# Kernel optimization log

Hardware: AMD Instinct MI355X
Metric: run time of the kernel (lower is better)

## Reference

```python
import jax, jax.numpy as jnp
import numpy as np

N_OBJ, N_SR, N_V, N_F = 8192, 4096, 4100, 4096
EPS = 1e-8


def setup_inputs() -> dict:
    key = jax.random.key(0)
    k1, k2, k3, k4, k5 = jax.random.split(key, 5)
    obj_points = jax.random.normal(k1, (N_OBJ, 3), jnp.float32)
    sr_points = 0.5 * jax.random.normal(k2, (N_SR, 3), jnp.float32)
    hand_verts = 0.5 * jax.random.normal(k3, (N_V, 3), jnp.float32)
    face_normals = jax.random.normal(k4, (N_F, 3), jnp.float32)
    hand_faces = jax.random.randint(k5, (N_F, 3), 0, N_V)
    return dict(obj_points=obj_points, sr_points=sr_points,
                hand_verts=hand_verts, face_normals=face_normals,
                hand_faces=hand_faces)


def reference(obj_points, sr_points, hand_verts, face_normals, hand_faces):
    # --- get_NN: brute-force nearest hand point for every object point ---
    d2 = (jnp.sum(obj_points**2, -1)[:, None]
          + jnp.sum(sr_points**2, -1)[None, :]
          - 2.0 * obj_points @ sr_points.T)          # [N, M] squared dists
    nn_idx = jnp.argmin(d2, axis=1)                   # [N]
    trg_pts = sr_points[nn_idx]                       # batched_index_select -> [N,3]
    D = trg_pts - obj_points                          # ray directions [N,3]

    # --- ray-triangle intersection (plane test + 3 edge half-plane tests) ---
    # All [F,N,3] intermediates are avoided via triple-product expansion:
    # every quantity reduces to einsums of per-face [F,3] with per-ray [N,3].
    tri = hand_verts[hand_faces]                      # [F,3,3]
    v0, v1, v2 = tri[:, 0], tri[:, 1], tri[:, 2]
    n = face_normals                                  # [F,3]

    denom = jnp.einsum('fk,nk->fn', n, D)             # D . n   [F,N]
    num = jnp.sum(v0 * n, -1)[:, None] - jnp.einsum('fk,nk->fn', n, obj_points)
    dmask = jnp.abs(denom) > EPS
    t = num / jnp.where(dmask, denom, 1.0)            # plane hit parameter [F,N]

    def edge_sign(va, vb):
        # ((vb-va) x (P-va)) . n  with  P = O + t*D, expanded bilinearly
        c = jnp.cross(n, vb - va)                     # [F,3]
        base = (jnp.einsum('fk,nk->fn', c, obj_points)
                - jnp.sum(va * c, -1)[:, None])
        return base + t * jnp.einsum('fk,nk->fn', c, D)

    inside = ((edge_sign(v0, v1) >= 0)
              & (edge_sign(v1, v2) >= 0)
              & (edge_sign(v2, v0) >= 0))
    hit = inside & dmask & (t > EPS)                  # [F,N]

    hit_number = jnp.sum(hit.astype(jnp.int32), axis=0)   # per ray [N]
    interior = (hit_number % 2) != 0                        # odd parity -> inside

    diff = trg_pts - obj_points
    pen_dist = jnp.sqrt(jnp.sum(diff**2 * interior[:, None].astype(diff.dtype)) + 1e-12)

    # --- contact_map_of_m_to_n(obj_points, sr_points) ---
    nn_dist = jnp.sqrt(jnp.maximum(jnp.min(d2, axis=1), 0.0))
    cmap = 1.0 - 2.0 * (jax.nn.sigmoid(100.0 * nn_dist) - 0.5)

    return pen_dist, cmap
```

## Files before the change

### kernel.cpp

```cpp
#include <hip/hip_runtime.h>
#include <math.h>

#define N_OBJ 8192
#define N_SR  4096
#define N_F   4096
#define EPSF  1e-8f
#define EPS2F 1e-16f

typedef float v2f __attribute__((ext_vector_type(2)));
static __device__ __forceinline__ v2f sp(float x) { v2f r; r.x = x; r.y = x; return r; }
static __device__ __forceinline__ v2f vfma(v2f a, v2f b, v2f c) { return __builtin_elementwise_fma(a, b, c); }

__global__ void __launch_bounds__(256) nn_all(const float* __restrict__ obj,
                                              const float* __restrict__ sr,
                                              const float* __restrict__ hv,
                                              const float* __restrict__ fn,
                                              const int* __restrict__ hf,
                                              float* __restrict__ out,
                                              float4* __restrict__ Dws,
                                              float4* __restrict__ F,
                                              int* __restrict__ done) {
    __shared__ float4 cXY[512];
    __shared__ float4 cZS[512];
    const int tid = threadIdx.x, b = blockIdx.x;
    const float2* sr2 = (const float2*)sr;

    if (b == 0 && tid == 0) done[0] = 0;
    if (tid < 4) {
        const int f = b * 4 + tid;
        const int i0 = hf[3*f], i1 = hf[3*f+1], i2 = hf[3*f+2];
        const float v0x = hv[3*i0], v0y = hv[3*i0+1], v0z = hv[3*i0+2];
        const float v1x = hv[3*i1], v1y = hv[3*i1+1], v1z = hv[3*i1+2];
        const float v2x = hv[3*i2], v2y = hv[3*i2+1], v2z = hv[3*i2+2];
        const float nx = fn[3*f], ny = fn[3*f+1], nz = fn[3*f+2];
        F[4*f+0] = make_float4(nx, ny, nz, v0x*nx + v0y*ny + v0z*nz);
        {
            float ex = v1x-v0x, ey = v1y-v0y, ez = v1z-v0z;
            float cx = ny*ez-nz*ey, cy = nz*ex-nx*ez, cz = nx*ey-ny*ex;
            F[4*f+1] = make_float4(cx, cy, cz, v0x*cx + v0y*cy + v0z*cz);
        }
        {
            float ex = v2x-v1x, ey = v2y-v1y, ez = v2z-v1z;
            float cx = ny*ez-nz*ey, cy = nz*ex-nx*ez, cz = nx*ey-ny*ex;
            F[4*f+2] = make_float4(cx, cy, cz, v1x*cx + v1y*cy + v1z*cz);
        }
        {
            float ex = v0x-v2x, ey = v0y-v2y, ez = v0z-v2z;
            float cx = ny*ez-nz*ey, cy = nz*ex-nx*ez, cz = nx*ey-ny*ex;
            F[4*f+3] = make_float4(cx, cy, cz, v2x*cx + v2y*cy + v2z*cz);
        }
    }

    const int w = tid >> 6, lane = tid & 63;
    const int p0 = b * 8 + w * 2, p1 = p0 + 1;

    const float ax = obj[3*p0], ay = obj[3*p0+1], az = obj[3*p0+2];
    const float bx = obj[3*p1], by = obj[3*p1+1], bz = obj[3*p1+2];
    const float aaa = fmaf(ax, ax, fmaf(ay, ay, az * az));
    const float aab = fmaf(bx, bx, fmaf(by, by, bz * bz));

    float a0 = INFINITY, a1 = INFINITY, c0v = INFINITY, c1v = INFINITY;
    int ai0 = 0, ai1 = 1, ci0 = 0, ci1 = 1;

    for (int c = 0; c < 4; ++c) {
        __syncthreads();
        {
#pragma unroll
            for (int t = 0; t < 2; ++t) {
                int e = t * 256 + tid;
                int gp = c * 512 + e;
                float2 A = sr2[3 * gp], B = sr2[3 * gp + 1], C = sr2[3 * gp + 2];
                float x0 = A.x, y0 = A.y, z0 = B.x, x1 = B.y, y1 = C.x, z1 = C.y;
                cXY[e] = make_float4(x0, x1, y0, y1);
                cZS[e] = make_float4(z0, z1,
                                     fmaf(x0, x0, fmaf(y0, y0, z0 * z0)),
                                     fmaf(x1, x1, fmaf(y1, y1, z1 * z1)));
            }
        }
        __syncthreads();

        int e2 = c * 1024 + lane * 2;
#pragma unroll
        for (int step = 0; step < 8; ++step) {
            int e = step * 64 + lane;
            float4 A = cXY[e];
            float4 B = cZS[e];
            v2f X; X.x = A.x; X.y = A.y;
            v2f Y; Y.x = A.z; Y.y = A.w;
            v2f Z; Z.x = B.x; Z.y = B.y;
            v2f SS; SS.x = B.z; SS.y = B.w;
            {
                v2f d  = vfma(Z, sp(az), vfma(Y, sp(ay), X * sp(ax)));
                v2f d2 = vfma(d, sp(-2.f), SS);
                bool q0 = d2.x < a0, q1 = d2.y < a1;
                a0 = q0 ? d2.x : a0;  ai0 = q0 ? e2     : ai0;
                a1 = q1 ? d2.y : a1;  ai1 = q1 ? e2 + 1 : ai1;
            }
            {
                v2f d  = vfma(Z, sp(bz), vfma(Y, sp(by), X * sp(bx)));
                v2f d2 = vfma(d, sp(-2.f), SS);
                bool q0 = d2.x < c0v, q1 = d2.y < c1v;
                c0v = q0 ? d2.x : c0v;  ci0 = q0 ? e2     : ci0;
                c1v = q1 ? d2.y : c1v;  ci1 = q1 ? e2 + 1 : ci1;
            }
            e2 += 128;
        }
    }

    float bdA = a0; int biA = ai0;
    if (a1 < bdA || (a1 == bdA && ai1 < biA)) { bdA = a1; biA = ai1; }
    float bdB = c0v; int biB = ci0;
    if (c1v < bdB || (c1v == bdB && ci1 < biB)) { bdB = c1v; biB = ci1; }
#pragma unroll
    for (int off = 32; off > 0; off >>= 1) {
        float d = __shfl_down(bdA, off);
        int   i = __shfl_down(biA, off);
        if (d < bdA || (d == bdA && i < biA)) { bdA = d; biA = i; }
        float e = __shfl_down(bdB, off);
        int   j = __shfl_down(biB, off);
        if (e < bdB || (e == bdB && j < biB)) { bdB = e; biB = j; }
    }
    if (lane == 0) {
        {
            float dx = sr[3*biA] - ax, dy = sr[3*biA+1] - ay, dz = sr[3*biA+2] - az;
            Dws[p0] = make_float4(dx, dy, dz, fmaf(dx, dx, fmaf(dy, dy, dz * dz)));
            float nn  = sqrtf(fmaxf(bdA + aaa, 0.f));
            float sig = 1.f / (1.f + expf(-100.f * nn));
            out[1 + p0] = 1.f - 2.f * (sig - 0.5f);
        }
        {
            float dx = sr[3*biB] - bx, dy = sr[3*biB+1] - by, dz = sr[3*biB+2] - bz;
            Dws[p1] = make_float4(dx, dy, dz, fmaf(dx, dx, fmaf(dy, dy, dz * dz)));
            float nn  = sqrtf(fmaxf(bdB + aab, 0.f));
            float sig = 1.f / (1.f + expf(-100.f * nn));
            out[1 + p1] = 1.f - 2.f * (sig - 0.5f);
        }
    }
}

#define RFC 64
#define RAY_NB 512
__global__ void __launch_bounds__(256) ray_count(const float* __restrict__ obj,
                                                 const float4* __restrict__ Dws,
                                                 const float4* __restrict__ F,
                                                 unsigned* __restrict__ pcount32,
                                                 int* __restrict__ done,
                                                 float* __restrict__ out) {
    __shared__ float4 sF[RFC * 4];
    __shared__ float wsum[4];
    __shared__ int lastf;
    const int tid = threadIdx.x;
    const int pg = blockIdx.x & 7, fc = blockIdx.x >> 3;

    sF[tid] = (F + (size_t)fc * RFC * 4)[tid];

    float px[4], py[4], pz[4], qx[4], qy[4], qz[4];
    int cnt[4];
    {
        const float4* obj4 = (const float4*)obj;
        int base = pg * 768 + tid * 3;
        float4 A = obj4[base], B = obj4[base + 1], C = obj4[base + 2];
        px[0] = A.x; py[0] = A.y; pz[0] = A.z;
        px[1] = A.w; py[1] = B.x; pz[1] = B.y;
        px[2] = B.z; py[2] = B.w; pz[2] = C.x;
        px[3] = C.y; py[3] = C.z; pz[3] = C.w;
        int p4 = pg * 1024 + tid * 4;
#pragma unroll
        for (int h = 0; h < 4; ++h) {
            float4 D = Dws[p4 + h];
            qx[h] = D.x; qy[h] = D.y; qz[h] = D.z;
            cnt[h] = 0;
        }
    }
    __syncthreads();

    float4 nF0 = sF[0], nF1 = sF[1], nF2 = sF[2], nF3 = sF[3];
#pragma unroll 4
    for (int f = 0; f < RFC; ++f) {
        const float4 Fn = nF0, C1 = nF1, C2 = nF2, C3 = nF3;
        if (f + 1 < RFC) {
            nF0 = sF[4*f+4]; nF1 = sF[4*f+5]; nF2 = sF[4*f+6]; nF3 = sF[4*f+7];
        }
#pragma unroll
        for (int h = 0; h < 4; ++h) {
            float denom = fmaf(Fn.z, qz[h], fmaf(Fn.y, qy[h], Fn.x * qx[h]));
            float num   = Fn.w - fmaf(Fn.z, pz[h], fmaf(Fn.y, py[h], Fn.x * px[h]));
            float d2 = denom * denom;
            float nd = num * denom;
            float wx = fmaf(px[h], d2, nd * qx[h]);
            float wy = fmaf(py[h], d2, nd * qy[h]);
            float wz = fmaf(pz[h], d2, nd * qz[h]);
            float q1 = fmaf(-C1.w, d2, fmaf(C1.z, wz, fmaf(C1.y, wy, C1.x * wx)));
            float q2 = fmaf(-C2.w, d2, fmaf(C2.z, wz, fmaf(C2.y, wy, C2.x * wx)));
            float q3 = fmaf(-C3.w, d2, fmaf(C3.z, wz, fmaf(C3.y, wy, C3.x * wx)));
            float tc = fmaf(-EPSF, d2, nd);
            float dc = d2 - EPS2F;
            float m  = fminf(fminf(q1, q2), fminf(q3, fminf(tc, dc)));
            cnt[h] += (m >= 0.f) ? 1 : 0;
        }
    }
    pcount32[(size_t)fc * 2048 + pg * 256 + tid] =
        (unsigned)cnt[0] | ((unsigned)cnt[1] << 8) |
        ((unsigned)cnt[2] << 16) | ((unsigned)cnt[3] << 24);

    __syncthreads();
    if (tid == 0) {
        __threadfence();
        lastf = (atomicAdd(done, 1) == RAY_NB - 1) ? 1 : 0;
    }
    __syncthreads();
    if (!lastf) return;
    __threadfence();

    float s = 0.f;
#pragma unroll
    for (int it = 0; it < 8; ++it) {
        int wi = it * 256 + tid;
        unsigned x = 0;
#pragma unroll 8
        for (int fcc = 0; fcc < 64; ++fcc)
            x ^= __hip_atomic_load(&pcount32[fcc * 2048 + wi],
                                   __ATOMIC_RELAXED, __HIP_MEMORY_SCOPE_AGENT);
        int p4 = wi * 4;
        if (x & 0x01u)        s += Dws[p4 + 0].w;
        if (x & 0x0100u)      s += Dws[p4 + 1].w;
        if (x & 0x010000u)    s += Dws[p4 + 2].w;
        if (x & 0x01000000u)  s += Dws[p4 + 3].w;
    }
#pragma unroll
    for (int off = 32; off > 0; off >>= 1) s += __shfl_down(s, off);
    if ((tid & 63) == 0) wsum[tid >> 6] = s;
    __syncthreads();
    if (tid == 0)
        out[0] = sqrtf(wsum[0] + wsum[1] + wsum[2] + wsum[3] + 1e-12f);
}

extern "C" void kernel_launch(void* const* d_in, const int* in_sizes, int n_in,
                              void* d_out, int out_size, void* d_ws, size_t ws_size,
                              hipStream_t stream) {
    const float* obj = (const float*)d_in[0];
    const float* sr  = (const float*)d_in[1];
    const float* hv  = (const float*)d_in[2];
    const float* fn  = (const float*)d_in[3];
    const int*   hf  = (const int*)d_in[4];
    float* out = (float*)d_out;

    char* ws = (char*)d_ws;
    float4*   Dws      = (float4*)(ws + 0);
    float4*   F        = (float4*)(ws + 131072);
    unsigned* pcount32 = (unsigned*)(ws + 393216);
    int*      done     = (int*)(ws + 917504);

    nn_all<<<1024, 256, 0, stream>>>(obj, sr, hv, fn, hf, out, Dws, F, done);
    ray_count<<<RAY_NB, 256, 0, stream>>>(obj, Dws, F, pcount32, done, out);
}
```

Baseline: 136.3 us.

## Split ray-count into more blocks and move parity reduction to separate finalize kernel

Halves the face chunk size so ray_count launches 1024 blocks instead of 512, giving more parallelism across CUs. The serial last-block reduction, in which a single block reads all per-chunk counts, is replaced by a separate 32-block finalize kernel that sums byte counts per point in parallel and combines the partial sums with an atomic counter. This adds a kernel launch and doubles the size of the partial-count buffer in exchange for removing the single-block tail.

Result: faster. 113.1 us (-17.0%).

```diff
diff --git a/kernel.cpp b/kernel.cpp
--- a/kernel.cpp
+++ b/kernel.cpp
@@ -138,21 +138,16 @@
     }
 }
 
-#define RFC 64
-#define RAY_NB 512
+#define RFC 32
 __global__ void __launch_bounds__(256) ray_count(const float* __restrict__ obj,
                                                  const float4* __restrict__ Dws,
                                                  const float4* __restrict__ F,
-                                                 unsigned* __restrict__ pcount32,
-                                                 int* __restrict__ done,
-                                                 float* __restrict__ out) {
+                                                 unsigned* __restrict__ pcount32) {
     __shared__ float4 sF[RFC * 4];
-    __shared__ float wsum[4];
-    __shared__ int lastf;
     const int tid = threadIdx.x;
     const int pg = blockIdx.x & 7, fc = blockIdx.x >> 3;
 
-    sF[tid] = (F + (size_t)fc * RFC * 4)[tid];
+    if (tid < RFC * 4) sF[tid] = (F + (size_t)fc * RFC * 4)[tid];
 
     float px[4], py[4], pz[4], qx[4], qy[4], qz[4];
     int cnt[4];
@@ -202,37 +197,37 @@
     pcount32[(size_t)fc * 2048 + pg * 256 + tid] =
         (unsigned)cnt[0] | ((unsigned)cnt[1] << 8) |
         ((unsigned)cnt[2] << 16) | ((unsigned)cnt[3] << 24);
-
-    __syncthreads();
-    if (tid == 0) {
-        __threadfence();
-        lastf = (atomicAdd(done, 1) == RAY_NB - 1) ? 1 : 0;
-    }
-    __syncthreads();
-    if (!lastf) return;
-    __threadfence();
-
-    float s = 0.f;
-#pragma unroll
-    for (int it = 0; it < 8; ++it) {
-        int wi = it * 256 + tid;
-        unsigned x = 0;
+}
+
+#define NCH (N_F / RFC)
+__global__ void __launch_bounds__(256) finalize(const float4* __restrict__ Dws,
+                                                const unsigned char* __restrict__ pcount,
+                                                float* __restrict__ fpart,
+                                                int* __restrict__ done,
+                                                float* __restrict__ out) {
+    __shared__ float wsum[4];
+    const int tid = threadIdx.x;
+    const int pt = blockIdx.x * 256 + tid;
+
+    int c = 0;
 #pragma unroll 8
-        for (int fcc = 0; fcc < 64; ++fcc)
-            x ^= __hip_atomic_load(&pcount32[fcc * 2048 + wi],
-                                   __ATOMIC_RELAXED, __HIP_MEMORY_SCOPE_AGENT);
-        int p4 = wi * 4;
-        if (x & 0x01u)        s += Dws[p4 + 0].w;
-        if (x & 0x0100u)      s += Dws[p4 + 1].w;
-        if (x & 0x010000u)    s += Dws[p4 + 2].w;
-        if (x & 0x01000000u)  s += Dws[p4 + 3].w;
-    }
+    for (int fc = 0; fc < NCH; ++fc)
+        c += pcount[(size_t)fc * N_OBJ + pt];
+    float s = (c & 1) ? Dws[pt].w : 0.f;
 #pragma unroll
     for (int off = 32; off > 0; off >>= 1) s += __shfl_down(s, off);
     if ((tid & 63) == 0) wsum[tid >> 6] = s;
     __syncthreads();
-    if (tid == 0)
-        out[0] = sqrtf(wsum[0] + wsum[1] + wsum[2] + wsum[3] + 1e-12f);
+    if (tid == 0) {
+        fpart[blockIdx.x] = wsum[0] + wsum[1] + wsum[2] + wsum[3];
+        __threadfence();
+        if (atomicAdd(done, 1) == 31) {
+            float tot = 0.f;
+            for (int i = 0; i < 32; ++i)
+                tot += atomicAdd(&fpart[i], 0.f);
+            out[0] = sqrtf(tot + 1e-12f);
+        }
+    }
 }
 
 extern "C" void kernel_launch(void* const* d_in, const int* in_sizes, int n_in,
@@ -249,8 +244,10 @@
     float4*   Dws      = (float4*)(ws + 0);
     float4*   F        = (float4*)(ws + 131072);
     unsigned* pcount32 = (unsigned*)(ws + 393216);
-    int*      done     = (int*)(ws + 917504);
+    float*    fpart    = (float*)(ws + 1441792);
+    int*      done     = (int*)(ws + 1441920);
 
     nn_all<<<1024, 256, 0, stream>>>(obj, sr, hv, fn, hf, out, Dws, F, done);
-    ray_count<<<RAY_NB, 256, 0, stream>>>(obj, Dws, F, pcount32, done, out);
-}
+    ray_count<<<1024, 256, 0, stream>>>(obj, Dws, F, pcount32);
+    finalize<<<32, 256, 0, stream>>>(Dws, (const unsigned char*)pcount32, fpart, done, out);
+}
```
